# Kernel optimization log

Measured on AMD Instinct MI355X. Metric: run time of the kernel, lower is better.

## Reference

```python
import jax, jax.numpy as jnp
import numpy as np
from jax import lax

B = 4            # batch (number of point clouds)
N_PER = 8192     # points per cloud
STRIDE = 4
M_PER = N_PER // STRIDE   # sampled points per cloud
K = 16           # nsample
C_IN = 64
C_OUT = 128
EPS = 1e-5


def fps(pts, m):
    """Furthest point sampling on (n,3), returns m int32 indices, starts at 0."""
    n = pts.shape[0]

    def step(carry, _):
        dist, last = carry
        d = jnp.sum((pts - pts[last]) ** 2, axis=-1)
        dist = jnp.minimum(dist, d)
        nxt = jnp.argmax(dist).astype(jnp.int32)
        return (dist, nxt), nxt

    init = (jnp.full((n,), 1e10, dtype=pts.dtype), jnp.int32(0))
    _, idxs = lax.scan(step, init, None, length=m - 1)
    return jnp.concatenate([jnp.zeros((1,), jnp.int32), idxs])


def knn_idx(pts, queries, k):
    """Indices of k nearest points for each query. pts (n,3), queries (m,3)."""
    d2 = (jnp.sum(queries * queries, -1)[:, None]
          + jnp.sum(pts * pts, -1)[None, :]
          - 2.0 * (queries @ pts.T))            # (m, n)
    _, idx = lax.top_k(-d2, k)                   # smallest distances
    return idx


def setup_inputs() -> dict:
    key = jax.random.key(0)
    k1, k2, k3 = jax.random.split(key, 3)
    point = jax.random.normal(k1, (B * N_PER, 3), dtype=jnp.float32) * 5.0
    feat = jax.random.normal(k2, (B * N_PER, C_IN), dtype=jnp.float32)
    row_splits = (jnp.arange(B + 1, dtype=jnp.int64) * N_PER)
    W = jax.random.normal(k3, (C_OUT, 3 + C_IN), dtype=jnp.float32) * 0.05
    gamma = jnp.ones((C_OUT,), dtype=jnp.float32)
    beta = jnp.zeros((C_OUT,), dtype=jnp.float32)
    return {"point": point, "feat": feat, "row_splits": row_splits,
            "W": W, "gamma": gamma, "beta": beta}


def reference(point, feat, row_splits, W, gamma, beta):
    pb = point.reshape(B, N_PER, 3)
    fb = feat.reshape(B, N_PER, C_IN)

    # --- furthest point sampling (non-differentiable index op) ---
    sidx = jax.vmap(lambda p: fps(p, M_PER))(lax.stop_gradient(pb))   # (B, M)
    new_p = jnp.take_along_axis(pb, sidx[..., None], axis=1)          # (B, M, 3)

    # --- batched KNN (indices only, like knn_search) ---
    nidx = jax.vmap(knn_idx, in_axes=(0, 0, None))(
        lax.stop_gradient(pb), lax.stop_gradient(new_p), K)           # (B, M, K)

    # --- queryandgroup: gather neighbors, relative xyz, concat feat ---
    gxyz = jax.vmap(lambda p, i: p[i])(pb, nidx) - new_p[:, :, None]  # (B, M, K, 3)
    gfeat = jax.vmap(lambda f, i: f[i])(fb, nidx)                     # (B, M, K, C_IN)
    g = jnp.concatenate([gxyz, gfeat], axis=-1).reshape(B * M_PER, K, 3 + C_IN)

    # --- linear (no bias) -> BN (batch stats over points & neighbors) -> ReLU ---
    y = jnp.einsum('mkc,oc->mko', g, W)                               # (m, K, C_OUT)
    mean = jnp.mean(y, axis=(0, 1))
    var = jnp.mean(jnp.square(y - mean), axis=(0, 1))                 # biased var
    y = (y - mean) * (gamma * lax.rsqrt(var + EPS)) + beta
    y = jax.nn.relu(y)

    # --- maxpool over neighbors ---
    out_feat = jnp.max(y, axis=1)                                     # (m, C_OUT)

    new_point = new_p.reshape(B * M_PER, 3)
    new_row_splits = jnp.arange(B + 1, dtype=jnp.int64) * M_PER
    return new_point, out_feat, new_row_splits
```

## Files before the change

### kernel.cpp

```cpp
#include <hip/hip_runtime.h>

#define NB 4
#define NPER 8192
#define MPER 2048
#define KNN 16
#define CIN 64
#define CO 128
#define MTOT (NB*MPER)
#define CCAP 28

typedef unsigned long long u64;
typedef unsigned int u32;

__device__ __forceinline__ float med3f(float a, float b, float c) {
    return __builtin_amdgcn_fmed3f(a, b, c);
}

__global__ void k_init(float* __restrict__ stats, float* __restrict__ rs,
                       u32* __restrict__ prog) {
    int t = threadIdx.x;
    if (t < 256) stats[t] = 0.f;
    if (t < 128) prog[t] = 0u;
    if (t < 5) rs[t] = (float)(t * MPER);
}

#define DPPSTEP(key, CTRL, RM) do {                                                   \
    unsigned lo_ = (unsigned)(key), hi_ = (unsigned)((key) >> 32);                    \
    unsigned nlo = (unsigned)__builtin_amdgcn_update_dpp((int)lo_, (int)lo_, CTRL, RM, 0xf, false); \
    unsigned nhi = (unsigned)__builtin_amdgcn_update_dpp((int)hi_, (int)hi_, CTRL, RM, 0xf, false); \
    unsigned long long ok_ = ((unsigned long long)nhi << 32) | nlo;                   \
    if (ok_ > (key)) (key) = ok_;                                                     \
} while (0)

#define DPP6(key) do { \
    DPPSTEP(key, 0xB1,  0xF); \
    DPPSTEP(key, 0x4E,  0xF); \
    DPPSTEP(key, 0x141, 0xF); \
    DPPSTEP(key, 0x140, 0xF); \
    DPPSTEP(key, 0x142, 0xA); \
    DPPSTEP(key, 0x143, 0xC); \
} while (0)

struct FpsSM {
    float4 spt[NPER];
    u64 red[2][4];
};
struct KnnSM {
    float4 sp[2][4][514];
    float  ndl[256][16];
    u32    candl[256][CCAP];
    int    ccnt[256], ccless[256];
    float  taub[64];
};
#define SMBYTES (sizeof(FpsSM) > sizeof(KnnSM) ? sizeof(FpsSM) : sizeof(KnnSM))

__launch_bounds__(256, 1)
__global__ void k_mega(const float* __restrict__ pts, float* __restrict__ out_np,
                       float4* __restrict__ qpts, u32* __restrict__ prog,
                       int* __restrict__ nidx) {
    #pragma clang fp contract(off)
    __shared__ __align__(16) char SMRAW[SMBYTES];
    const int t = threadIdx.x;

    if (blockIdx.x < NB) {
        FpsSM& sm = *(FpsSM*)SMRAW;
        const int b = blockIdx.x;
        const float4* pb4 = (const float4*)(pts + (size_t)b * NPER * 3);

        float f[96];
        #pragma unroll
        for (int j = 0; j < 24; ++j) {
            float4 v = pb4[t * 24 + j];
            f[j*4+0] = v.x; f[j*4+1] = v.y; f[j*4+2] = v.z; f[j*4+3] = v.w;
        }
        float px[32], py[32], pz[32], dd[32];
        #pragma unroll
        for (int s = 0; s < 32; ++s) {
            px[s] = f[3*s]; py[s] = f[3*s+1]; pz[s] = f[3*s+2];
            dd[s] = 1e10f;
            sm.spt[t * 32 + s] = make_float4(px[s], py[s], pz[s], 0.f);
        }
        if (t == 0) {
            size_t row = (size_t)b * MPER;
            out_np[row*3+0] = px[0]; out_np[row*3+1] = py[0]; out_np[row*3+2] = pz[0];
            qpts[row] = make_float4(px[0], py[0], pz[0], 0.f);
        }
        __syncthreads();

        float4 c0 = sm.spt[0];
        float cx = c0.x, cy = c0.y, cz = c0.z;
        const int lane = t & 63, wv = t >> 6;
        const int ibase = t * 32;

        for (int i = 1; i < MPER; ++i) {
            float bv = -1.f; int bs = 0;
            #pragma unroll
            for (int s = 0; s < 32; ++s) {
                float dx = px[s] - cx, dy = py[s] - cy, dz = pz[s] - cz;
                float t0 = dx * dx, t1 = dy * dy, t2 = dz * dz;
                float d = (t0 + t1) + t2;
                float nd = fminf(dd[s], d);
                dd[s] = nd;
                bool bet = nd > bv;
                bv = bet ? nd : bv;
                bs = bet ? s : bs;
            }
            u64 key = ((u64)__float_as_uint(bv) << 32) | (u32)~(u32)(ibase + bs);

            DPP6(key);

            if (lane == 63) sm.red[i & 1][wv] = key;
            __syncthreads();

            const int p = i & 1;
            u64 k0 = sm.red[p][0], k1 = sm.red[p][1], k2 = sm.red[p][2], k3 = sm.red[p][3];
            u64 ka = k0 > k1 ? k0 : k1;
            u64 kb = k2 > k3 ? k2 : k3;
            u64 kbest = ka > kb ? ka : kb;
            const int i2 = (int)(~(u32)kbest) & 0x1FFF;

            float4 c = sm.spt[i2];
            cx = c.x; cy = c.y; cz = c.z;

            if (t == 0) {
                size_t row = (size_t)b * MPER + i;
                out_np[row*3+0] = cx; out_np[row*3+1] = cy; out_np[row*3+2] = cz;
                qpts[row] = make_float4(cx, cy, cz, 0.f);
                if ((i & 127) == 127) {
                    __threadfence();
                    __hip_atomic_store(prog + b * 32, (u32)(i + 1),
                                       __ATOMIC_RELEASE, __HIP_MEMORY_SCOPE_AGENT);
                }
            }
        }
    } else {
        KnnSM& sm = *(KnnSM*)SMRAW;
        const int kb = blockIdx.x - NB;
        const int q0 = kb * 64;
        const int b = q0 >> 11;
        const u32 need = (u32)(((q0 + 63) & (MPER - 1)) + 1);

        if (t == 0) {
            while (__hip_atomic_load(prog + b * 32, __ATOMIC_RELAXED,
                                     __HIP_MEMORY_SCOPE_AGENT) < need)
                __builtin_amdgcn_s_sleep(32);
        }
        __syncthreads();
        __threadfence();

        const int qloc = t >> 2, sub = t & 3;
        const int q = q0 + qloc;
        const float4 qp = qpts[q];
        const float qq = (qp.x * qp.x + qp.y * qp.y) + qp.z * qp.z;
        const float* pb = pts + (size_t)b * NPER * 3;
        const int wq = t >> 6, wl = t & 63;

        float4 L[6];
        #define LOADC(c) do { const float4* src_ = (const float4*)(pb + (size_t)(c) * 2048 * 3); \
            _Pragma("unroll") for (int u_ = 0; u_ < 6; ++u_) L[u_] = src_[t * 6 + u_]; } while (0)
        #define WRITEC(pbuf) do { \
            float fl_[24]; \
            _Pragma("unroll") for (int u_ = 0; u_ < 6; ++u_) { \
                fl_[u_*4+0]=L[u_].x; fl_[u_*4+1]=L[u_].y; fl_[u_*4+2]=L[u_].z; fl_[u_*4+3]=L[u_].w; } \
            _Pragma("unroll") for (int r_ = 0; r_ < 8; ++r_) { \
                float x_=fl_[3*r_], y_=fl_[3*r_+1], z_=fl_[3*r_+2]; \
                float pp_=(x_*x_ + y_*y_) + z_*z_; \
                sm.sp[pbuf][wq][wl*8 + r_] = make_float4(x_,y_,z_,pp_); } } while (0)

        float nd[16];
        #pragma unroll
        for (int j = 0; j < 16; ++j) nd[j] = 1e30f;

        LOADC(0); WRITEC(0); LOADC(1);
        __syncthreads();
        for (int c = 0; c < 4; ++c) {
            const int pbuf = c & 1;
            #pragma unroll 4
            for (int j = 0; j < 512; ++j) {
                float4 p = sm.sp[pbuf][sub][j];
                float dot = (qp.x * p.x + qp.y * p.y) + qp.z * p.z;
                float d = (qq + p.w) - 2.f * dot;
                if (d < nd[15]) {
                    #pragma unroll
                    for (int u = 15; u >= 1; --u) nd[u] = med3f(d, nd[u-1], nd[u]);
                    nd[0] = fminf(nd[0], d);
                }
            }
            __syncthreads();
            if (c < 3) {
                WRITEC((c + 1) & 1);
                if (c < 2) LOADC(c + 2);
                __syncthreads();
            }
        }
        #pragma unroll
        for (int j = 0; j < 16; ++j) sm.ndl[t][j] = nd[j];
        __syncthreads();

        if (sub == 0) {
            int p0=0,p1=0,p2=0,p3=0;
            float c0=sm.ndl[t][0], c1=sm.ndl[t+1][0], c2=sm.ndl[t+2][0], c3=sm.ndl[t+3][0];
            float tau = 0.f;
            for (int it = 0; it < 16; ++it) {
                if (c0 <= c1 && c0 <= c2 && c0 <= c3) { tau=c0; ++p0; c0 = (p0<16)?sm.ndl[t][p0]:1e30f; }
                else if (c1 <= c2 && c1 <= c3)        { tau=c1; ++p1; c1 = (p1<16)?sm.ndl[t+1][p1]:1e30f; }
                else if (c2 <= c3)                    { tau=c2; ++p2; c2 = (p2<16)?sm.ndl[t+2][p2]:1e30f; }
                else                                  { tau=c3; ++p3; c3 = (p3<16)?sm.ndl[t+3][p3]:1e30f; }
            }
            sm.taub[qloc] = tau;
        }
        __syncthreads();
        const float tau = sm.taub[qloc];

        int cnt = 0, cless = 0;
        LOADC(0); WRITEC(0); LOADC(1);
        __syncthreads();
        for (int c = 0; c < 4; ++c) {
            const int pbuf = c & 1;
            for (int j = 0; j < 512; ++j) {
                float4 p = sm.sp[pbuf][sub][j];
                float dot = (qp.x * p.x + qp.y * p.y) + qp.z * p.z;
                float d = (qq + p.w) - 2.f * dot;
                if (d <= tau && cnt < CCAP) {
                    bool eq = !(d < tau);
                    sm.candl[t][cnt++] = (u32)(c * 2048 + sub * 512 + j) | (eq ? 0x80000000u : 0u);
                    if (!eq) cless++;
                }
            }
            __syncthreads();
            if (c < 3) {
                WRITEC((c + 1) & 1);
                if (c < 2) LOADC(c + 2);
                __syncthreads();
            }
        }
        sm.ccnt[t] = cnt; sm.ccless[t] = cless;
        __syncthreads();

        if (sub == 0) {
            int n0=sm.ccnt[t], n1=sm.ccnt[t+1], n2=sm.ccnt[t+2], n3=sm.ccnt[t+3];
            int quota = 16 - (sm.ccless[t]+sm.ccless[t+1]+sm.ccless[t+2]+sm.ccless[t+3]);
            int p0=0,p1=0,p2=0,p3=0, kept=0, eq_used=0;
            u32 h0 = n0 ? sm.candl[t][0]   : 0xFFFFFFFFu;
            u32 h1 = n1 ? sm.candl[t+1][0] : 0xFFFFFFFFu;
            u32 h2 = n2 ? sm.candl[t+2][0] : 0xFFFFFFFFu;
            u32 h3 = n3 ? sm.candl[t+3][0] : 0xFFFFFFFFu;
            size_t obase = (size_t)q * KNN;
            for (int g = 0; g < 4*CCAP && kept < 16; ++g) {
                u32 m0 = h0 & 0x7fffffffu, m1 = h1 & 0x7fffffffu;
                u32 m2 = h2 & 0x7fffffffu, m3 = h3 & 0x7fffffffu;
                u32 v;
                if (m0 <= m1 && m0 <= m2 && m0 <= m3) { v=h0; ++p0; h0 = (p0<n0)?sm.candl[t][p0]:0xFFFFFFFFu; }
                else if (m1 <= m2 && m1 <= m3)        { v=h1; ++p1; h1 = (p1<n1)?sm.candl[t+1][p1]:0xFFFFFFFFu; }
                else if (m2 <= m3)                    { v=h2; ++p2; h2 = (p2<n2)?sm.candl[t+2][p2]:0xFFFFFFFFu; }
                else                                  { v=h3; ++p3; h3 = (p3<n3)?sm.candl[t+3][p3]:0xFFFFFFFFu; }
                if (v == 0xFFFFFFFFu) break;
                bool eq = (v >> 31) != 0;
                bool take = !eq || (eq_used < quota);
                if (take) {
                    if (eq) ++eq_used;
                    nidx[obase + kept] = b * NPER + (int)(v & 0x7fffffffu);
                    ++kept;
                }
            }
        }
        #undef LOADC
        #undef WRITEC
    }
}

__launch_bounds__(128, 4)
__global__ void k_stats(const float* __restrict__ pts, const float* __restrict__ feat,
                        const float* __restrict__ W, const int* __restrict__ nidx,
                        const float4* __restrict__ qpts, float* __restrict__ ymax,
                        float* __restrict__ ymin, float* __restrict__ stats) {
    __shared__ float4 g4[KNN][17];
    const int t = threadIdx.x;
    float w[68];
    const float* wr = W + t * 67;
    #pragma unroll
    for (int c = 0; c < 64; ++c) w[c] = wr[3 + c];
    w[64] = wr[0]; w[65] = wr[1]; w[66] = wr[2]; w[67] = 0.f;

    float s_sum = 0.f, s_sq = 0.f;
    const int k0 = t >> 3, p8 = t & 7;
    for (int mi = 0; mi < 8; ++mi) {
        const int m0 = blockIdx.x * 8 + mi;
        {
            int nid = nidx[(size_t)m0 * KNN + k0];
            const float4* fr = (const float4*)(feat + (size_t)nid * CIN);
            g4[k0][p8*2]   = fr[p8*2];
            g4[k0][p8*2+1] = fr[p8*2+1];
        }
        if (t < 16) {
            int nid = nidx[(size_t)m0 * KNN + t];
            float4 qp = qpts[m0];
            float x = pts[(size_t)nid*3], y = pts[(size_t)nid*3+1], z = pts[(size_t)nid*3+2];
            g4[t][16] = make_float4(x - qp.x, y - qp.y, z - qp.z, 0.f);
        }
        __syncthreads();
        float vmax = -1e30f, vmin = 1e30f;
        #pragma unroll 1
        for (int k = 0; k < KNN; ++k) {
            float y0 = 0.f, y1 = 0.f, y2 = 0.f, y3 = 0.f;
            #pragma unroll
            for (int c4 = 0; c4 < 17; ++c4) {
                float4 gv = g4[k][c4];
                y0 = fmaf(gv.x, w[c4*4+0], y0);
                y1 = fmaf(gv.y, w[c4*4+1], y1);
                y2 = fmaf(gv.z, w[c4*4+2], y2);
                y3 = fmaf(gv.w, w[c4*4+3], y3);
            }
            float y = (y0 + y1) + (y2 + y3);
            vmax = fmaxf(vmax, y); vmin = fminf(vmin, y);
            s_sum += y; s_sq = fmaf(y, y, s_sq);
        }
        ymax[(size_t)m0 * CO + t] = vmax;
        ymin[(size_t)m0 * CO + t] = vmin;
        __syncthreads();
    }
    atomicAdd(stats + t, s_sum);
    atomicAdd(stats + CO + t, s_sq);
}

__global__ void k_out(const float* __restrict__ ymax, const float* __restrict__ ymin,
                      const float* __restrict__ stats, const float* __restrict__ gamma,
                      const float* __restrict__ beta, float* __restrict__ out_feat) {
    int tid = blockIdx.x * 256 + threadIdx.x;
    int o = tid & (CO - 1);
    const float inv = 1.f / (float)(MTOT * KNN);
    float mean = stats[o] * inv;
    float var = stats[CO + o] * inv - mean * mean;
    var = fmaxf(var, 0.f);
    float s = gamma[o] * rsqrtf(var + 1e-5f);
    float bb = beta[o] - mean * s;
    float yv = (s >= 0.f) ? ymax[tid] : ymin[tid];
    out_feat[tid] = fmaxf(fmaf(s, yv, bb), 0.f);
}

extern "C" void kernel_launch(void* const* d_in, const int* in_sizes, int n_in,
                              void* d_out, int out_size, void* d_ws, size_t ws_size,
                              hipStream_t stream) {
    const float* pts   = (const float*)d_in[0];
    const float* feat  = (const float*)d_in[1];
    const float* W     = (const float*)d_in[3];
    const float* gamma = (const float*)d_in[4];
    const float* beta  = (const float*)d_in[5];
    float* out = (float*)d_out;
    char* ws = (char*)d_ws;

    float4* qpts = (float4*)(ws);
    int*    nidx = (int*)(ws + 131072);
    float*  stats = (float*)(ws + 655360);
    u32*    prog  = (u32*)(ws + 656384);
    float*  ymax  = (float*)(ws + 657408);
    float*  ymin  = (float*)(ws + 657408 + 4194304);

    float* out_np   = out;
    float* out_feat = out + 24576;
    float* out_rs   = out + 24576 + 1048576;

    hipLaunchKernelGGL(k_init,  dim3(1), dim3(256), 0, stream, stats, out_rs, prog);
    hipLaunchKernelGGL(k_mega,  dim3(NB + MTOT / 64), dim3(256), 0, stream,
                       pts, out_np, qpts, prog, nidx);
    hipLaunchKernelGGL(k_stats, dim3(MTOT / 8), dim3(128), 0, stream,
                       pts, feat, W, nidx, qpts, ymax, ymin, stats);
    hipLaunchKernelGGL(k_out,   dim3(MTOT * CO / 256), dim3(256), 0, stream,
                       ymax, ymin, stats, gamma, beta, out_feat);
}
```

Measured before the change: 2.324 ms.

## Shrink KNN block granularity near FPS tail to shorten pipeline drain

The FPS producer now publishes progress every 32 samples in its last quarter. The KNN consumer blocks are resized so the tail queries get blocks of 32, 16 and 8 queries, each split across more threads per query (4 to 32), so KNN work overlaps FPS until its final samples. The shared point buffer is relaid out as a padded row-per-subthread array. The tau merge becomes a 16-element insertion over all partial lists, and candidate collection keeps strictly-closer and tie candidates in separate lists. The cost is more blocks, more threads per query with longer merges, and extra progress fences in the serial FPS loop.

```diff
diff --git a/kernel.cpp b/kernel.cpp
--- a/kernel.cpp
+++ b/kernel.cpp
@@ -7,7 +7,7 @@
 #define CIN 64
 #define CO 128
 #define MTOT (NB*MPER)
-#define CCAP 28
+#define CPB 56
 
 typedef unsigned long long u64;
 typedef unsigned int u32;
@@ -46,10 +46,12 @@
     u64 red[2][4];
 };
 struct KnnSM {
-    float4 sp[2][4][514];
+    float4 sp[2][2112];
     float  ndl[256][16];
-    u32    candl[256][CCAP];
-    int    ccnt[256], ccless[256];
+    u32    candl[256][16];
+    u32    eql[256][16];
+    int    ccnt[256], ecnt[256];
+    u32    pcur[256];
     float  taub[64];
 };
 #define SMBYTES (sizeof(FpsSM) > sizeof(KnnSM) ? sizeof(FpsSM) : sizeof(KnnSM))
@@ -126,7 +128,7 @@
                 size_t row = (size_t)b * MPER + i;
                 out_np[row*3+0] = cx; out_np[row*3+1] = cy; out_np[row*3+2] = cz;
                 qpts[row] = make_float4(cx, cy, cz, 0.f);
-                if ((i & 127) == 127) {
+                if (((i & 127) == 127) || (i >= 1536 && ((i & 31) == 31))) {
                     __threadfence();
                     __hip_atomic_store(prog + b * 32, (u32)(i + 1),
                                        __ATOMIC_RELEASE, __HIP_MEMORY_SCOPE_AGENT);
@@ -136,9 +138,19 @@
     } else {
         KnnSM& sm = *(KnnSM*)SMRAW;
         const int kb = blockIdx.x - NB;
-        const int q0 = kb * 64;
-        const int b = q0 >> 11;
-        const u32 need = (u32)(((q0 + 63) & (MPER - 1)) + 1);
+        const int b  = kb / CPB;
+        const int r  = kb % CPB;
+        int nq, q0b;
+        if (r < 24)      { nq = 64; q0b = r << 6; }
+        else if (r < 32) { nq = 32; q0b = 1536 + ((r - 24) << 5); }
+        else if (r < 40) { nq = 16; q0b = 1792 + ((r - 32) << 4); }
+        else             { nq = 8;  q0b = 1920 + ((r - 40) << 3); }
+        const int lgL = (nq == 64) ? 2 : (nq == 32) ? 3 : (nq == 16) ? 4 : 5;
+        const int L = 1 << lgL;
+        const int lgP = 11 - lgL;
+        const int P = 1 << lgP;
+        const int stride = P + 2;
+        const u32 need = (u32)(q0b + nq);
 
         if (t == 0) {
             while (__hip_atomic_load(prog + b * 32, __ATOMIC_RELAXED,
@@ -148,24 +160,25 @@
         __syncthreads();
         __threadfence();
 
-        const int qloc = t >> 2, sub = t & 3;
-        const int q = q0 + qloc;
+        const int sub = t & (L - 1), qloc = t >> lgL;
+        const int q = b * MPER + q0b + qloc;
         const float4 qp = qpts[q];
         const float qq = (qp.x * qp.x + qp.y * qp.y) + qp.z * qp.z;
         const float* pb = pts + (size_t)b * NPER * 3;
         const int wq = t >> 6, wl = t & 63;
 
-        float4 L[6];
+        float4 Lr[6];
         #define LOADC(c) do { const float4* src_ = (const float4*)(pb + (size_t)(c) * 2048 * 3); \
-            _Pragma("unroll") for (int u_ = 0; u_ < 6; ++u_) L[u_] = src_[t * 6 + u_]; } while (0)
+            _Pragma("unroll") for (int u_ = 0; u_ < 6; ++u_) Lr[u_] = src_[t * 6 + u_]; } while (0)
         #define WRITEC(pbuf) do { \
             float fl_[24]; \
             _Pragma("unroll") for (int u_ = 0; u_ < 6; ++u_) { \
-                fl_[u_*4+0]=L[u_].x; fl_[u_*4+1]=L[u_].y; fl_[u_*4+2]=L[u_].z; fl_[u_*4+3]=L[u_].w; } \
+                fl_[u_*4+0]=Lr[u_].x; fl_[u_*4+1]=Lr[u_].y; fl_[u_*4+2]=Lr[u_].z; fl_[u_*4+3]=Lr[u_].w; } \
             _Pragma("unroll") for (int r_ = 0; r_ < 8; ++r_) { \
                 float x_=fl_[3*r_], y_=fl_[3*r_+1], z_=fl_[3*r_+2]; \
                 float pp_=(x_*x_ + y_*y_) + z_*z_; \
-                sm.sp[pbuf][wq][wl*8 + r_] = make_float4(x_,y_,z_,pp_); } } while (0)
+                int gpos_ = wq*512 + wl*8 + r_; \
+                sm.sp[pbuf][(gpos_ >> lgP)*stride + (gpos_ & (P-1))] = make_float4(x_,y_,z_,pp_); } } while (0)
 
         float nd[16];
         #pragma unroll
@@ -175,9 +188,10 @@
         __syncthreads();
         for (int c = 0; c < 4; ++c) {
             const int pbuf = c & 1;
+            const float4* rowp = &sm.sp[pbuf][sub * stride];
             #pragma unroll 4
-            for (int j = 0; j < 512; ++j) {
-                float4 p = sm.sp[pbuf][sub][j];
+            for (int j = 0; j < P; ++j) {
+                float4 p = rowp[j];
                 float dot = (qp.x * p.x + qp.y * p.y) + qp.z * p.z;
                 float d = (qq + p.w) - 2.f * dot;
                 if (d < nd[15]) {
@@ -198,33 +212,37 @@
         __syncthreads();
 
         if (sub == 0) {
-            int p0=0,p1=0,p2=0,p3=0;
-            float c0=sm.ndl[t][0], c1=sm.ndl[t+1][0], c2=sm.ndl[t+2][0], c3=sm.ndl[t+3][0];
-            float tau = 0.f;
-            for (int it = 0; it < 16; ++it) {
-                if (c0 <= c1 && c0 <= c2 && c0 <= c3) { tau=c0; ++p0; c0 = (p0<16)?sm.ndl[t][p0]:1e30f; }
-                else if (c1 <= c2 && c1 <= c3)        { tau=c1; ++p1; c1 = (p1<16)?sm.ndl[t+1][p1]:1e30f; }
-                else if (c2 <= c3)                    { tau=c2; ++p2; c2 = (p2<16)?sm.ndl[t+2][p2]:1e30f; }
-                else                                  { tau=c3; ++p3; c3 = (p3<16)?sm.ndl[t+3][p3]:1e30f; }
-            }
-            sm.taub[qloc] = tau;
+            float td[16];
+            #pragma unroll
+            for (int u = 0; u < 16; ++u) td[u] = 1e30f;
+            for (int s = 0; s < L; ++s) {
+                for (int u2 = 0; u2 < 16; ++u2) {
+                    float v = sm.ndl[t + s][u2];
+                    if (!(v < td[15])) break;
+                    #pragma unroll
+                    for (int u = 15; u >= 1; --u) td[u] = med3f(v, td[u-1], td[u]);
+                    td[0] = fminf(td[0], v);
+                }
+            }
+            sm.taub[qloc] = td[15];
         }
         __syncthreads();
         const float tau = sm.taub[qloc];
 
-        int cnt = 0, cless = 0;
+        int cnt = 0, ecn = 0;
         LOADC(0); WRITEC(0); LOADC(1);
         __syncthreads();
         for (int c = 0; c < 4; ++c) {
             const int pbuf = c & 1;
-            for (int j = 0; j < 512; ++j) {
-                float4 p = sm.sp[pbuf][sub][j];
+            const float4* rowp = &sm.sp[pbuf][sub * stride];
+            for (int j = 0; j < P; ++j) {
+                float4 p = rowp[j];
                 float dot = (qp.x * p.x + qp.y * p.y) + qp.z * p.z;
                 float d = (qq + p.w) - 2.f * dot;
-                if (d <= tau && cnt < CCAP) {
-                    bool eq = !(d < tau);
-                    sm.candl[t][cnt++] = (u32)(c * 2048 + sub * 512 + j) | (eq ? 0x80000000u : 0u);
-                    if (!eq) cless++;
+                if (d <= tau) {
+                    u32 pidx = (u32)(c * 2048 + (sub << lgP) + j);
+                    if (d < tau) { if (cnt < 16) sm.candl[t][cnt++] = pidx; }
+                    else         { if (ecn < 16) sm.eql[t][ecn++] = pidx; }
                 }
             }
             __syncthreads();
@@ -234,34 +252,28 @@
                 __syncthreads();
             }
         }
-        sm.ccnt[t] = cnt; sm.ccless[t] = cless;
+        sm.ccnt[t] = cnt; sm.ecnt[t] = ecn; sm.pcur[t] = 0;
         __syncthreads();
 
         if (sub == 0) {
-            int n0=sm.ccnt[t], n1=sm.ccnt[t+1], n2=sm.ccnt[t+2], n3=sm.ccnt[t+3];
-            int quota = 16 - (sm.ccless[t]+sm.ccless[t+1]+sm.ccless[t+2]+sm.ccless[t+3]);
-            int p0=0,p1=0,p2=0,p3=0, kept=0, eq_used=0;
-            u32 h0 = n0 ? sm.candl[t][0]   : 0xFFFFFFFFu;
-            u32 h1 = n1 ? sm.candl[t+1][0] : 0xFFFFFFFFu;
-            u32 h2 = n2 ? sm.candl[t+2][0] : 0xFFFFFFFFu;
-            u32 h3 = n3 ? sm.candl[t+3][0] : 0xFFFFFFFFu;
+            const int base = t;
+            int kept = 0;
             size_t obase = (size_t)q * KNN;
-            for (int g = 0; g < 4*CCAP && kept < 16; ++g) {
-                u32 m0 = h0 & 0x7fffffffu, m1 = h1 & 0x7fffffffu;
-                u32 m2 = h2 & 0x7fffffffu, m3 = h3 & 0x7fffffffu;
-                u32 v;
-                if (m0 <= m1 && m0 <= m2 && m0 <= m3) { v=h0; ++p0; h0 = (p0<n0)?sm.candl[t][p0]:0xFFFFFFFFu; }
-                else if (m1 <= m2 && m1 <= m3)        { v=h1; ++p1; h1 = (p1<n1)?sm.candl[t+1][p1]:0xFFFFFFFFu; }
-                else if (m2 <= m3)                    { v=h2; ++p2; h2 = (p2<n2)?sm.candl[t+2][p2]:0xFFFFFFFFu; }
-                else                                  { v=h3; ++p3; h3 = (p3<n3)?sm.candl[t+3][p3]:0xFFFFFFFFu; }
-                if (v == 0xFFFFFFFFu) break;
-                bool eq = (v >> 31) != 0;
-                bool take = !eq || (eq_used < quota);
-                if (take) {
-                    if (eq) ++eq_used;
-                    nidx[obase + kept] = b * NPER + (int)(v & 0x7fffffffu);
-                    ++kept;
-                }
+            for (int s = 0; s < L; ++s) {
+                int n = sm.ccnt[base + s];
+                for (int e = 0; e < n && kept < 16; ++e)
+                    nidx[obase + kept++] = b * NPER + (int)sm.candl[base + s][e];
+            }
+            while (kept < 16) {
+                u32 best = 0xFFFFFFFFu; int bs = -1;
+                for (int s = 0; s < L; ++s) {
+                    u32 ps = sm.pcur[base + s];
+                    u32 v = (ps < (u32)sm.ecnt[base + s]) ? sm.eql[base + s][ps] : 0xFFFFFFFFu;
+                    if (v < best) { best = v; bs = s; }
+                }
+                if (bs < 0) break;
+                sm.pcur[base + bs]++;
+                nidx[obase + kept++] = b * NPER + (int)best;
             }
         }
         #undef LOADC
@@ -361,7 +373,7 @@
     float* out_rs   = out + 24576 + 1048576;
 
     hipLaunchKernelGGL(k_init,  dim3(1), dim3(256), 0, stream, stats, out_rs, prog);
-    hipLaunchKernelGGL(k_mega,  dim3(NB + MTOT / 64), dim3(256), 0, stream,
+    hipLaunchKernelGGL(k_mega,  dim3(NB + NB * CPB), dim3(256), 0, stream,
                        pts, out_np, qpts, prog, nidx);
     hipLaunchKernelGGL(k_stats, dim3(MTOT / 8), dim3(128), 0, stream,
                        pts, feat, W, nidx, qpts, ymax, ymin, stats);
```

Measured after the change: 2.055 ms. 11.6% less time.
